# Kernel tuning notes

Measured on AMD Instinct MI355X. Metric: run time of the kernel, lower is better.

Reference implementation:

```python
import jax, jax.numpy as jnp
import numpy as np

# ---- static config (mirrors PointRend init kwargs) ----
H, W = 512, 512          # img_size
CH, CW = 128, 128        # coarse_size
FH, FW = 256, 256        # fine_size
CF = 256                 # fine_channels
NC = 3                   # num_classes (forced by MLP's hard-coded 259/131 channel counts)
NPTS = 2048              # N points
K_OVER = 3               # k oversampling
BELTA = 0.75
NUM_OVER = K_OVER * NPTS          # 6144
STEP1 = int(NPTS * BELTA)         # 1536 uncertain points
STEP2 = NPTS - STEP1              # 512 coverage points


def _xavier(key, c_out, c_in):
    std = (2.0 / (c_in + c_out)) ** 0.5
    return jax.random.normal(key, (c_out, c_in), jnp.float32) * std


def setup_inputs() -> dict:
    key = jax.random.key(0)
    k1, k2, k3, k4, k5, k6 = jax.random.split(key, 6)
    fine_grained = jax.random.normal(k1, (2, CF, FH, FW), jnp.float32)
    coarse_pre = jax.random.normal(k2, (2, NC, CH, CW), jnp.float32)
    # torch.randperm(H*W) done inside forward in the original; passed in for determinism
    random_1d_index = jax.random.permutation(k3, H * W).astype(jnp.int32)
    w1 = _xavier(k4, 256, CF + NC)   # conv1: 1x1, in=259, out=256, no bias
    w2 = _xavier(k5, 128, 256 + 3)   # conv2: in=259, out=128
    w3 = _xavier(k6, NC, 128 + 3)    # conv3: in=131, out=num_classes
    prelu_a = jnp.array(0.25, jnp.float32)  # shared single-param PReLU
    return dict(fine_grained=fine_grained, coarse_pre=coarse_pre,
                w1=w1, w2=w2, w3=w3, prelu_a=prelu_a,
                random_1d_index=random_1d_index)


def _bilinear(x, h, w):
    # matches nn.Upsample(mode='bilinear', align_corners=False)
    return jax.image.resize(x, (x.shape[0], x.shape[1], h, w), method="bilinear")


def _prelu(x, a):
    return jnp.where(x >= 0, x, a * x)


def _mlp(feat, w1, w2, w3, a):
    # feat: [B, N, C] -> channels-first [B, C, N]; BatchNorms in MLP are unused in forward.
    x = jnp.transpose(feat, (0, 2, 1))
    tail = x[:, -3:, :]  # last 3 channels appended to each layer's input
    l1 = _prelu(jnp.einsum('bcn,oc->bon', x, w1), a)
    l2 = _prelu(jnp.einsum('bcn,oc->bon', jnp.concatenate([l1, tail], 1), w2), a)
    return jnp.einsum('bcn,oc->bon', jnp.concatenate([l2, tail], 1), w3)  # [B, NC, N]


def reference(fine_grained, coarse_pre, w1, w2, w3, prelu_a, random_1d_index):
    B = fine_grained.shape[0]
    up_coarse_o = _bilinear(coarse_pre, H, W)            # [B, NC, H, W] logits
    up_coarse_sm = jax.nn.softmax(up_coarse_o, axis=1)   # softmax over classes
    up_fine = _bilinear(fine_grained, H, W)              # [B, CF, H, W]

    h_idx = random_1d_index // W
    w_idx = random_1d_index % W
    all_index = jnp.stack([h_idx, w_idx], axis=1)        # [H*W, 2]
    cand = all_index[:NUM_OVER]                          # oversampled candidates

    # vectorized replacement of the python loop: gather probs at candidates
    over_pre = up_coarse_sm[:, :, cand[:, 0], cand[:, 1]].transpose(0, 2, 1)  # [B, NUM_OVER, NC]
    top2, _ = jax.lax.top_k(over_pre, 2)
    uncertain = 1.0 - (top2[..., 0] - top2[..., 1])      # [B, NUM_OVER]
    _, u_idx = jax.lax.top_k(uncertain, STEP1)           # [B, STEP1]
    u_pts = cand[u_idx]                                  # [B, STEP1, 2]
    cov = jnp.broadcast_to(all_index[-STEP2:][None], (B, STEP2, 2))
    pts = jnp.concatenate([u_pts, cov], axis=1)          # [B, N, 2]

    # masked_select traverses the dense mask in row-major (h,w) order -> sort linear ids
    lin = pts[..., 0] * W + pts[..., 1]                  # [B, N]
    lin_sorted = jnp.sort(lin, axis=1)
    sh, sw = lin_sorted // W, lin_sorted % W
    bidx = jnp.arange(B)[:, None]
    sel_coarse = up_coarse_o[bidx, :, sh, sw]            # [B, N, NC] (pre-softmax feats)
    sel_fine = up_fine[bidx, :, sh, sw]                  # [B, N, CF]

    # faithful to torch: flat concat of the two masked_select outputs, then reshape
    feat = jnp.concatenate([sel_fine.reshape(-1), sel_coarse.reshape(-1)]).reshape(B, NPTS, -1)

    out = _mlp(feat, w1, w2, w3, prelu_a)                # [B, NC, N]
    mask = jnp.zeros((B, H, W), jnp.int32).at[bidx, pts[..., 0], pts[..., 1]].add(1)
    return out, mask
```

## Files before the change

### kernel.cpp

```cpp
#include <hip/hip_runtime.h>

#define NPTS 2048
#define NOVER 6144
#define STEP1 1536
#define STEP2 512
#define HW_TOT 262144

__device__ __forceinline__ float prelu_f(float x, float a) { return x >= 0.0f ? x : a * x; }

__device__ __forceinline__ void coarse_coords(int h, int w, float& fy, float& fx,
                                              int& y0, int& y1, int& x0, int& x1) {
  float sy = (h + 0.5f) * 0.25f - 0.5f;
  float sx = (w + 0.5f) * 0.25f - 0.5f;
  float yf = floorf(sy), xf = floorf(sx);
  fy = sy - yf; fx = sx - xf;
  int yi = (int)yf, xi = (int)xf;
  y0 = min(127, max(0, yi)); y1 = min(127, max(0, yi + 1));
  x0 = min(127, max(0, xi)); x1 = min(127, max(0, xi + 1));
}

__device__ __forceinline__ float coarse_sample(const float* __restrict__ ch, float fy, float fx,
                                               int y0, int y1, int x0, int x1) {
  float v00 = ch[(y0 << 7) + x0];
  float v01 = ch[(y0 << 7) + x1];
  float v10 = ch[(y1 << 7) + x0];
  float v11 = ch[(y1 << 7) + x1];
  return (1.0f - fy) * ((1.0f - fx) * v00 + fx * v01) + fy * ((1.0f - fx) * v10 + fx * v11);
}

__global__ __launch_bounds__(256) void pr_uncfill_v9(uint4* __restrict__ mask4,
                                                     const float* __restrict__ coarse,
                                                     const int* __restrict__ ridx,
                                                     unsigned* __restrict__ keys) {
  const int bb = blockIdx.x;
  if (bb < 512) {
    mask4[bb * 256 + threadIdx.x] = make_uint4(0u, 0u, 0u, 0u);
    return;
  }
  int gid = (bb - 512) * 256 + threadIdx.x;
  if (gid >= 2 * NOVER) return;
  int b = gid / NOVER, i = gid - b * NOVER;
  int lin = ridx[i];
  int h = lin >> 9, w = lin & 511;
  float fy, fx; int y0, y1, x0, x1;
  coarse_coords(h, w, fy, fx, y0, y1, x0, x1);
  const float* cb = coarse + (((size_t)b * 3) << 14);
  float p0 = coarse_sample(cb, fy, fx, y0, y1, x0, x1);
  float p1 = coarse_sample(cb + (1 << 14), fy, fx, y0, y1, x0, x1);
  float p2 = coarse_sample(cb + (2 << 14), fy, fx, y0, y1, x0, x1);
  float m = fmaxf(p0, fmaxf(p1, p2));
  float e0 = expf(p0 - m), e1 = expf(p1 - m), e2 = expf(p2 - m);
  float s = e0 + e1 + e2;
  float q0 = e0 / s, q1 = e1 / s, q2 = e2 / s;
  float a0 = q0, a1 = q1, a2 = q2, tmp;
  if (a0 < a1) { tmp = a0; a0 = a1; a1 = tmp; }
  if (a1 < a2) { tmp = a1; a1 = a2; a2 = tmp; }
  if (a0 < a1) { tmp = a0; a0 = a1; a1 = tmp; }
  float u = 1.0f - (a0 - a1);
  keys[gid] = __float_as_uint(u);
}

__global__ __launch_bounds__(256) void pr_wprep_v4(const float* __restrict__ w1,
                                                   const float* __restrict__ w2,
                                                   float* __restrict__ wT1,
                                                   float* __restrict__ wT2) {
  int gid = blockIdx.x * 256 + threadIdx.x;
  if (gid < 259 * 256) {
    int c = gid >> 8, o = gid & 255;
    wT1[c * 256 + o] = w1[o * 259 + c];
  } else {
    int g2 = gid - 259 * 256;
    if (g2 < 259 * 128) {
      int c = g2 >> 7, o = g2 & 127;
      wT2[c * 128 + o] = w2[o * 259 + c];
    }
  }
}

__global__ __launch_bounds__(1024) void pr_topk_v4(const unsigned* __restrict__ keys,
                                                   const int* __restrict__ ridx,
                                                   int* __restrict__ lin_sorted,
                                                   float* __restrict__ mask) {
  __shared__ unsigned kv[NOVER];
  __shared__ unsigned bitmap[8192];
  __shared__ unsigned hist[256];
  __shared__ unsigned short tiebuf[NOVER];
  __shared__ unsigned scanbuf[16];
  __shared__ unsigned selinfo[2];
  __shared__ int tiecnt;
  const int b = blockIdx.x, t = threadIdx.x;
  const int lane = t & 63, wid = t >> 6;

  for (int i = t; i < NOVER; i += 1024) kv[i] = keys[b * NOVER + i];
  for (int i = t; i < 8192; i += 1024) bitmap[i] = 0u;
  if (t == 0) { selinfo[1] = STEP1; tiecnt = 0; }
  __syncthreads();

  unsigned prefix = 0u;
  for (int pass = 0; pass < 4; ++pass) {
    const int shift = 24 - 8 * pass;
    const unsigned maskHi = (pass == 0) ? 0u : (0xFFFFFFFFu << (shift + 8));
    for (int i = t; i < 256; i += 1024) hist[i] = 0u;
    __syncthreads();
    for (int i = t; i < NOVER; i += 1024) {
      unsigned k = kv[i];
      if ((k & maskHi) == prefix) atomicAdd(&hist[(k >> shift) & 255u], 1u);
    }
    __syncthreads();
    if (t < 64) {
      unsigned h0 = hist[t * 4], h1 = hist[t * 4 + 1], h2 = hist[t * 4 + 2], h3 = hist[t * 4 + 3];
      unsigned q = h0 + h1 + h2 + h3;
      unsigned s = q;
      for (int off = 1; off < 64; off <<= 1) {
        unsigned n = __shfl_down(s, off);
        if (t + off < 64) s += n;
      }
      unsigned exq = s - q;
      unsigned R = selinfo[1];
      unsigned se3 = exq, se2 = se3 + h3, se1 = se2 + h2, se0 = se1 + h1;
      if (se3 < R && R <= se3 + h3)      { selinfo[0] = prefix | ((unsigned)(t * 4 + 3) << shift); selinfo[1] = R - se3; }
      else if (se2 < R && R <= se2 + h2) { selinfo[0] = prefix | ((unsigned)(t * 4 + 2) << shift); selinfo[1] = R - se2; }
      else if (se1 < R && R <= se1 + h1) { selinfo[0] = prefix | ((unsigned)(t * 4 + 1) << shift); selinfo[1] = R - se1; }
      else if (se0 < R && R <= se0 + h0) { selinfo[0] = prefix | ((unsigned)(t * 4 + 0) << shift); selinfo[1] = R - se0; }
    }
    __syncthreads();
    prefix = selinfo[0];
  }
  const unsigned T = prefix;
  const int r = (int)selinfo[1];

  for (int i = t; i < NOVER; i += 1024) {
    unsigned k = kv[i];
    if (k > T) {
      int lin = ridx[i];
      mask[(size_t)b * HW_TOT + lin] = 1.0f;
      atomicOr(&bitmap[lin >> 5], 1u << (lin & 31));
    } else if (k == T) {
      int pos = atomicAdd(&tiecnt, 1);
      tiebuf[pos] = (unsigned short)i;
    }
  }
  for (int i = t; i < STEP2; i += 1024) {
    int lin = ridx[HW_TOT - STEP2 + i];
    mask[(size_t)b * HW_TOT + lin] = 1.0f;
    atomicOr(&bitmap[lin >> 5], 1u << (lin & 31));
  }
  __syncthreads();
  const int m = tiecnt;
  for (int j = t; j < m; j += 1024) {
    int idx = tiebuf[j];
    int rank = 0;
    for (int jj = 0; jj < m; ++jj) rank += (tiebuf[jj] < idx) ? 1 : 0;
    if (rank < r) {
      int lin = ridx[idx];
      mask[(size_t)b * HW_TOT + lin] = 1.0f;
      atomicOr(&bitmap[lin >> 5], 1u << (lin & 31));
    }
  }
  __syncthreads();

  unsigned mySum = 0;
#pragma unroll
  for (int q = 0; q < 8; ++q) mySum += __popc(bitmap[t * 8 + q]);
  unsigned v = mySum;
  for (int off = 1; off < 64; off <<= 1) {
    unsigned n = __shfl_up(v, off);
    if (lane >= off) v += n;
  }
  if (lane == 63) scanbuf[wid] = v;
  __syncthreads();
  if (t == 0) {
    unsigned run = 0;
    for (int w16 = 0; w16 < 16; ++w16) { unsigned tmp = scanbuf[w16]; scanbuf[w16] = run; run += tmp; }
  }
  __syncthreads();
  unsigned pos = (v - mySum) + scanbuf[wid];
  for (int q = 0; q < 8; ++q) {
    unsigned word = bitmap[t * 8 + q];
    int basebit = (t * 8 + q) << 5;
    while (word) {
      int bit = __ffs(word) - 1;
      word &= word - 1;
      lin_sorted[b * NPTS + pos++] = basebit + bit;
    }
  }
}

__global__ __launch_bounds__(256) void pr_gather_v9(const float* __restrict__ fine,
                                                    const float* __restrict__ coarse,
                                                    const int* __restrict__ lin_sorted,
                                                    float* __restrict__ fv,
                                                    float* __restrict__ cv) {
  const int tid = blockIdx.x * 256 + threadIdx.x;
  if (tid < 1048576) {
    const int s = tid & 4095, ch = tid >> 12;
    const int bs = s >> 11;
    const int lin = lin_sorted[s];
    const int h = lin >> 9, w = lin & 511;
    float sy = (h + 0.5f) * 0.5f - 0.5f;
    float sx = (w + 0.5f) * 0.5f - 0.5f;
    float yf = floorf(sy), xf = floorf(sx);
    float fy = sy - yf, fx = sx - xf;
    int yi = (int)yf, xi = (int)xf;
    int y0 = min(255, max(0, yi)), y1 = min(255, max(0, yi + 1));
    int x0 = min(255, max(0, xi)), x1 = min(255, max(0, xi + 1));
    const float* base = fine + (((size_t)(bs * 256 + ch)) << 16);
    float v00 = base[(y0 << 8) + x0];
    float v01 = base[(y0 << 8) + x1];
    float v10 = base[(y1 << 8) + x0];
    float v11 = base[(y1 << 8) + x1];
    fv[tid] = (1.0f - fy) * ((1.0f - fx) * v00 + fx * v01)
            + fy * ((1.0f - fx) * v10 + fx * v11);
  } else {
    const int u = tid - 1048576;
    const int s = u & 4095, kk = u >> 12;
    const int bs = s >> 11;
    const int lin = lin_sorted[s];
    const int h = lin >> 9, w = lin & 511;
    float fy, fx; int y0, y1, x0, x1;
    coarse_coords(h, w, fy, fx, y0, y1, x0, x1);
    cv[u] = coarse_sample(coarse + (((size_t)bs * 3 + kk) << 14), fy, fx, y0, y1, x0, x1);
  }
}

__global__ __launch_bounds__(512) void pr_mlpc_v10(const float* __restrict__ fv,
                                                   const float* __restrict__ cv,
                                                   const float* __restrict__ wT1,
                                                   const float* __restrict__ wT2,
                                                   const float* __restrict__ w3,
                                                   const float* __restrict__ pa,
                                                   float* __restrict__ out) {
  __shared__ __align__(16) float wbuf[2][8192];
  __shared__ __align__(16) float xs[259][16];
  __shared__ __align__(16) float l1p[16][260];
  __shared__ __align__(16) float l2p[16][132];
  const int t = threadIdx.x;
  const int lane = t & 63, wid = t >> 6;
  const int g0 = blockIdx.x * 16;
  const float a = pa[0];

  const int ob1 = ((wid & 3) << 6) + ((lane & 15) << 2);
  const int pp1 = ((wid >> 2) << 3) + ((lane >> 4) << 1);
  const int ob2 = (t & 31) * 4;
  const int pt2 = t >> 5;

  float4 t1[3], t2[3];
#pragma unroll
  for (int i = 0; i < 3; ++i) {
    t1[i] = *(const float4*)&wT1[(256 + i) * 256 + ob1];
    t2[i] = *(const float4*)&wT2[(256 + i) * 128 + ob2];
  }
  float4 st[4];
#pragma unroll
  for (int j = 0; j < 4; ++j) st[j] = *(const float4*)&wT1[(j * 512 + t) * 4];

  for (int task = t; task < 259 * 16; task += 512) {
    int c = task >> 4, p = task & 15;
    int j = (g0 + p) * 259 + c;
    float v;
    if (j < 1048576) {
      v = fv[(j & 255) * 4096 + (j >> 8)];
    } else {
      int jj = j - 1048576;
      int nsrc = jj / 3, kk = jj - nsrc * 3;
      v = cv[kk * 4096 + nsrc];
    }
    xs[c][p] = v;
  }
#pragma unroll
  for (int j = 0; j < 4; ++j) *(float4*)&wbuf[0][(j * 512 + t) * 4] = st[j];
  __syncthreads();

  float acc1[4][2];
#pragma unroll
  for (int i = 0; i < 4; ++i) { acc1[i][0] = 0.0f; acc1[i][1] = 0.0f; }
  float acc2[4] = {0.0f, 0.0f, 0.0f, 0.0f};

  for (int k = 0; k < 12; ++k) {
    const int cur = k & 1;
    if (k < 11) {
      const float* src;
      if (k < 7)       src = wT1 + (k + 1) * 8192;
      else if (k == 7) src = wT2;
      else             src = wT2 + (k - 7) * 8192;
#pragma unroll
      for (int j = 0; j < 4; ++j) st[j] = *(const float4*)&src[(j * 512 + t) * 4];
    }

    if (k < 8) {
      const float* w = wbuf[cur];
      const int c0 = k * 32;
#pragma unroll 8
      for (int cl = 0; cl < 32; ++cl) {
        const float4 wv = *(const float4*)&w[cl * 256 + ob1];
        const float2 xv = *(const float2*)&xs[c0 + cl][pp1];
        acc1[0][0] = fmaf(wv.x, xv.x, acc1[0][0]); acc1[0][1] = fmaf(wv.x, xv.y, acc1[0][1]);
        acc1[1][0] = fmaf(wv.y, xv.x, acc1[1][0]); acc1[1][1] = fmaf(wv.y, xv.y, acc1[1][1]);
        acc1[2][0] = fmaf(wv.z, xv.x, acc1[2][0]); acc1[2][1] = fmaf(wv.z, xv.y, acc1[2][1]);
        acc1[3][0] = fmaf(wv.w, xv.x, acc1[3][0]); acc1[3][1] = fmaf(wv.w, xv.y, acc1[3][1]);
      }
      if (k == 7) {
#pragma unroll
        for (int i = 0; i < 3; ++i) {
          const float2 xv = *(const float2*)&xs[256 + i][pp1];
          acc1[0][0] = fmaf(t1[i].x, xv.x, acc1[0][0]); acc1[0][1] = fmaf(t1[i].x, xv.y, acc1[0][1]);
          acc1[1][0] = fmaf(t1[i].y, xv.x, acc1[1][0]); acc1[1][1] = fmaf(t1[i].y, xv.y, acc1[1][1]);
          acc1[2][0] = fmaf(t1[i].z, xv.x, acc1[2][0]); acc1[2][1] = fmaf(t1[i].z, xv.y, acc1[2][1]);
          acc1[3][0] = fmaf(t1[i].w, xv.x, acc1[3][0]); acc1[3][1] = fmaf(t1[i].w, xv.y, acc1[3][1]);
        }
#pragma unroll
        for (int q = 0; q < 2; ++q) {
          float4 o;
          o.x = prelu_f(acc1[0][q], a);
          o.y = prelu_f(acc1[1][q], a);
          o.z = prelu_f(acc1[2][q], a);
          o.w = prelu_f(acc1[3][q], a);
          *(float4*)&l1p[pp1 + q][ob1] = o;
        }
      }
    } else {
      const float* w = wbuf[cur];
      const int c0 = (k - 8) * 64;
#pragma unroll 4
      for (int cl = 0; cl < 64; cl += 4) {
        const float4 xv = *(const float4*)&l1p[pt2][c0 + cl];
        const float4 w0 = *(const float4*)&w[(cl + 0) * 128 + ob2];
        const float4 w1v = *(const float4*)&w[(cl + 1) * 128 + ob2];
        const float4 w2v = *(const float4*)&w[(cl + 2) * 128 + ob2];
        const float4 w3v = *(const float4*)&w[(cl + 3) * 128 + ob2];
        acc2[0] = fmaf(w0.x, xv.x, acc2[0]); acc2[1] = fmaf(w0.y, xv.x, acc2[1]);
        acc2[2] = fmaf(w0.z, xv.x, acc2[2]); acc2[3] = fmaf(w0.w, xv.x, acc2[3]);
        acc2[0] = fmaf(w1v.x, xv.y, acc2[0]); acc2[1] = fmaf(w1v.y, xv.y, acc2[1]);
        acc2[2] = fmaf(w1v.z, xv.y, acc2[2]); acc2[3] = fmaf(w1v.w, xv.y, acc2[3]);
        acc2[0] = fmaf(w2v.x, xv.z, acc2[0]); acc2[1] = fmaf(w2v.y, xv.z, acc2[1]);
        acc2[2] = fmaf(w2v.z, xv.z, acc2[2]); acc2[3] = fmaf(w2v.w, xv.z, acc2[3]);
        acc2[0] = fmaf(w3v.x, xv.w, acc2[0]); acc2[1] = fmaf(w3v.y, xv.w, acc2[1]);
        acc2[2] = fmaf(w3v.z, xv.w, acc2[2]); acc2[3] = fmaf(w3v.w, xv.w, acc2[3]);
      }
      if (k == 11) {
#pragma unroll
        for (int i = 0; i < 3; ++i) {
          const float x0 = xs[256 + i][pt2];
          acc2[0] = fmaf(t2[i].x, x0, acc2[0]); acc2[1] = fmaf(t2[i].y, x0, acc2[1]);
          acc2[2] = fmaf(t2[i].z, x0, acc2[2]); acc2[3] = fmaf(t2[i].w, x0, acc2[3]);
        }
        float4 o;
        o.x = prelu_f(acc2[0], a);
        o.y = prelu_f(acc2[1], a);
        o.z = prelu_f(acc2[2], a);
        o.w = prelu_f(acc2[3], a);
        *(float4*)&l2p[pt2][ob2] = o;
      }
    }

    if (k < 11) {
#pragma unroll
      for (int j = 0; j < 4; ++j) *(float4*)&wbuf[cur ^ 1][(j * 512 + t) * 4] = st[j];
    }
    __syncthreads();
  }

  if (t < 48) {
    const int o3 = t % 3, p = t / 3;
    const float* wr = w3 + o3 * 131;
    float s = 0.0f;
#pragma unroll 4
    for (int c = 0; c < 128; ++c) s = fmaf(wr[c], l2p[p][c], s);
#pragma unroll
    for (int kk = 0; kk < 3; ++kk) s = fmaf(wr[128 + kk], xs[256 + kk][p], s);
    const int g = g0 + p;
    out[((g >> 11) * 3 + o3) * 2048 + (g & 2047)] = s;
  }
}

extern "C" void kernel_launch(void* const* d_in, const int* in_sizes, int n_in,
                              void* d_out, int out_size, void* d_ws, size_t ws_size,
                              hipStream_t stream) {
  const float* fine   = (const float*)d_in[0];
  const float* coarse = (const float*)d_in[1];
  const float* w1     = (const float*)d_in[2];
  const float* w2     = (const float*)d_in[3];
  const float* w3     = (const float*)d_in[4];
  const float* pa     = (const float*)d_in[5];
  const int*   ridx   = (const int*)d_in[6];

  float* out  = (float*)d_out;
  float* mask = out + 2 * 3 * 2048;

  char* ws = (char*)d_ws;
  int*      lin_sorted = (int*)ws;
  float*    wT1  = (float*)(ws + 16384);
  float*    wT2  = (float*)(ws + 281600);
  unsigned* keys = (unsigned*)(ws + 414208);
  float*    fv   = (float*)(ws + 463360);
  float*    cv   = (float*)(ws + 4657664);

  pr_uncfill_v9<<<560, 256, 0, stream>>>((uint4*)mask, coarse, ridx, keys);
  pr_wprep_v4<<<389, 256, 0, stream>>>(w1, w2, wT1, wT2);
  pr_topk_v4<<<2, 1024, 0, stream>>>(keys, ridx, lin_sorted, mask);
  pr_gather_v9<<<4144, 256, 0, stream>>>(fine, coarse, lin_sorted, fv, cv);
  pr_mlpc_v10<<<256, 512, 0, stream>>>(fv, cv, wT1, wT2, w3, pa, out);
}
```

Before: 280.3 us.

## Fuse bilinear gather into MLP kernel and merge prep kernels

Removes the separate gather kernel and its intermediate fv/cv buffers: the MLP kernel now samples fine and coarse features bilinearly straight into shared memory, with loads batched across 9 iterations per thread to keep many requests in flight. The mask-clear/uncertainty and weight-transpose kernels are merged into a single launch. This drops two launches and a roughly 4 MB write-then-read round trip, but the gather now runs inside only 256 blocks with heavier register use, so memory-level parallelism for the scattered fine-feature reads may be lower.

```diff
diff --git a/kernel.cpp b/kernel.cpp
--- a/kernel.cpp
+++ b/kernel.cpp
@@ -28,43 +28,44 @@
   return (1.0f - fy) * ((1.0f - fx) * v00 + fx * v01) + fy * ((1.0f - fx) * v10 + fx * v11);
 }
 
-__global__ __launch_bounds__(256) void pr_uncfill_v9(uint4* __restrict__ mask4,
-                                                     const float* __restrict__ coarse,
-                                                     const int* __restrict__ ridx,
-                                                     unsigned* __restrict__ keys) {
+__global__ __launch_bounds__(256) void pr_prep_v11(uint4* __restrict__ mask4,
+                                                   const float* __restrict__ coarse,
+                                                   const int* __restrict__ ridx,
+                                                   unsigned* __restrict__ keys,
+                                                   const float* __restrict__ w1,
+                                                   const float* __restrict__ w2,
+                                                   float* __restrict__ wT1,
+                                                   float* __restrict__ wT2) {
   const int bb = blockIdx.x;
   if (bb < 512) {
     mask4[bb * 256 + threadIdx.x] = make_uint4(0u, 0u, 0u, 0u);
     return;
   }
-  int gid = (bb - 512) * 256 + threadIdx.x;
-  if (gid >= 2 * NOVER) return;
-  int b = gid / NOVER, i = gid - b * NOVER;
-  int lin = ridx[i];
-  int h = lin >> 9, w = lin & 511;
-  float fy, fx; int y0, y1, x0, x1;
-  coarse_coords(h, w, fy, fx, y0, y1, x0, x1);
-  const float* cb = coarse + (((size_t)b * 3) << 14);
-  float p0 = coarse_sample(cb, fy, fx, y0, y1, x0, x1);
-  float p1 = coarse_sample(cb + (1 << 14), fy, fx, y0, y1, x0, x1);
-  float p2 = coarse_sample(cb + (2 << 14), fy, fx, y0, y1, x0, x1);
-  float m = fmaxf(p0, fmaxf(p1, p2));
-  float e0 = expf(p0 - m), e1 = expf(p1 - m), e2 = expf(p2 - m);
-  float s = e0 + e1 + e2;
-  float q0 = e0 / s, q1 = e1 / s, q2 = e2 / s;
-  float a0 = q0, a1 = q1, a2 = q2, tmp;
-  if (a0 < a1) { tmp = a0; a0 = a1; a1 = tmp; }
-  if (a1 < a2) { tmp = a1; a1 = a2; a2 = tmp; }
-  if (a0 < a1) { tmp = a0; a0 = a1; a1 = tmp; }
-  float u = 1.0f - (a0 - a1);
-  keys[gid] = __float_as_uint(u);
-}
-
-__global__ __launch_bounds__(256) void pr_wprep_v4(const float* __restrict__ w1,
-                                                   const float* __restrict__ w2,
-                                                   float* __restrict__ wT1,
-                                                   float* __restrict__ wT2) {
-  int gid = blockIdx.x * 256 + threadIdx.x;
+  if (bb < 560) {
+    int gid = (bb - 512) * 256 + threadIdx.x;
+    if (gid >= 2 * NOVER) return;
+    int b = gid / NOVER, i = gid - b * NOVER;
+    int lin = ridx[i];
+    int h = lin >> 9, w = lin & 511;
+    float fy, fx; int y0, y1, x0, x1;
+    coarse_coords(h, w, fy, fx, y0, y1, x0, x1);
+    const float* cb = coarse + (((size_t)b * 3) << 14);
+    float p0 = coarse_sample(cb, fy, fx, y0, y1, x0, x1);
+    float p1 = coarse_sample(cb + (1 << 14), fy, fx, y0, y1, x0, x1);
+    float p2 = coarse_sample(cb + (2 << 14), fy, fx, y0, y1, x0, x1);
+    float m = fmaxf(p0, fmaxf(p1, p2));
+    float e0 = expf(p0 - m), e1 = expf(p1 - m), e2 = expf(p2 - m);
+    float s = e0 + e1 + e2;
+    float q0 = e0 / s, q1 = e1 / s, q2 = e2 / s;
+    float a0 = q0, a1 = q1, a2 = q2, tmp;
+    if (a0 < a1) { tmp = a0; a0 = a1; a1 = tmp; }
+    if (a1 < a2) { tmp = a1; a1 = a2; a2 = tmp; }
+    if (a0 < a1) { tmp = a0; a0 = a1; a1 = tmp; }
+    float u = 1.0f - (a0 - a1);
+    keys[gid] = __float_as_uint(u);
+    return;
+  }
+  int gid = (bb - 560) * 256 + threadIdx.x;
   if (gid < 259 * 256) {
     int c = gid >> 8, o = gid & 255;
     wT1[c * 256 + o] = w1[o * 259 + c];
@@ -186,50 +187,14 @@
   }
 }
 
-__global__ __launch_bounds__(256) void pr_gather_v9(const float* __restrict__ fine,
+__global__ __launch_bounds__(512) void pr_fused_v11(const float* __restrict__ fine,
                                                     const float* __restrict__ coarse,
                                                     const int* __restrict__ lin_sorted,
-                                                    float* __restrict__ fv,
-                                                    float* __restrict__ cv) {
-  const int tid = blockIdx.x * 256 + threadIdx.x;
-  if (tid < 1048576) {
-    const int s = tid & 4095, ch = tid >> 12;
-    const int bs = s >> 11;
-    const int lin = lin_sorted[s];
-    const int h = lin >> 9, w = lin & 511;
-    float sy = (h + 0.5f) * 0.5f - 0.5f;
-    float sx = (w + 0.5f) * 0.5f - 0.5f;
-    float yf = floorf(sy), xf = floorf(sx);
-    float fy = sy - yf, fx = sx - xf;
-    int yi = (int)yf, xi = (int)xf;
-    int y0 = min(255, max(0, yi)), y1 = min(255, max(0, yi + 1));
-    int x0 = min(255, max(0, xi)), x1 = min(255, max(0, xi + 1));
-    const float* base = fine + (((size_t)(bs * 256 + ch)) << 16);
-    float v00 = base[(y0 << 8) + x0];
-    float v01 = base[(y0 << 8) + x1];
-    float v10 = base[(y1 << 8) + x0];
-    float v11 = base[(y1 << 8) + x1];
-    fv[tid] = (1.0f - fy) * ((1.0f - fx) * v00 + fx * v01)
-            + fy * ((1.0f - fx) * v10 + fx * v11);
-  } else {
-    const int u = tid - 1048576;
-    const int s = u & 4095, kk = u >> 12;
-    const int bs = s >> 11;
-    const int lin = lin_sorted[s];
-    const int h = lin >> 9, w = lin & 511;
-    float fy, fx; int y0, y1, x0, x1;
-    coarse_coords(h, w, fy, fx, y0, y1, x0, x1);
-    cv[u] = coarse_sample(coarse + (((size_t)bs * 3 + kk) << 14), fy, fx, y0, y1, x0, x1);
-  }
-}
-
-__global__ __launch_bounds__(512) void pr_mlpc_v10(const float* __restrict__ fv,
-                                                   const float* __restrict__ cv,
-                                                   const float* __restrict__ wT1,
-                                                   const float* __restrict__ wT2,
-                                                   const float* __restrict__ w3,
-                                                   const float* __restrict__ pa,
-                                                   float* __restrict__ out) {
+                                                    const float* __restrict__ wT1,
+                                                    const float* __restrict__ wT2,
+                                                    const float* __restrict__ w3,
+                                                    const float* __restrict__ pa,
+                                                    float* __restrict__ out) {
   __shared__ __align__(16) float wbuf[2][8192];
   __shared__ __align__(16) float xs[259][16];
   __shared__ __align__(16) float l1p[16][260];
@@ -254,18 +219,56 @@
 #pragma unroll
   for (int j = 0; j < 4; ++j) st[j] = *(const float4*)&wT1[(j * 512 + t) * 4];
 
-  for (int task = t; task < 259 * 16; task += 512) {
-    int c = task >> 4, p = task & 15;
-    int j = (g0 + p) * 259 + c;
-    float v;
-    if (j < 1048576) {
-      v = fv[(j & 255) * 4096 + (j >> 8)];
-    } else {
-      int jj = j - 1048576;
-      int nsrc = jj / 3, kk = jj - nsrc * 3;
-      v = cv[kk * 4096 + nsrc];
-    }
-    xs[c][p] = v;
+  float v00[9], v01[9], v10[9], v11[9], gfy[9], gfx[9];
+#pragma unroll
+  for (int it = 0; it < 9; ++it) {
+    const int task = t + it * 512;
+    if (task < 4144) {
+      const int c = task >> 4, p = task & 15;
+      const int j = (g0 + p) * 259 + c;
+      if (j < 1048576) {
+        const int nsrc = j >> 8, ch = j & 255;
+        const int bs = nsrc >> 11;
+        const int lin = lin_sorted[nsrc];
+        const int h = lin >> 9, w = lin & 511;
+        float sy = (h + 0.5f) * 0.5f - 0.5f;
+        float sx = (w + 0.5f) * 0.5f - 0.5f;
+        float yf = floorf(sy), xf = floorf(sx);
+        gfy[it] = sy - yf; gfx[it] = sx - xf;
+        int yi = (int)yf, xi = (int)xf;
+        int y0 = min(255, max(0, yi)), y1 = min(255, max(0, yi + 1));
+        int x0 = min(255, max(0, xi)), x1 = min(255, max(0, xi + 1));
+        const float* base = fine + (((size_t)(bs * 256 + ch)) << 16);
+        v00[it] = base[(y0 << 8) + x0];
+        v01[it] = base[(y0 << 8) + x1];
+        v10[it] = base[(y1 << 8) + x0];
+        v11[it] = base[(y1 << 8) + x1];
+      } else {
+        const int jj = j - 1048576;
+        const int nsrc = jj / 3, kk = jj - nsrc * 3;
+        const int bs = nsrc >> 11;
+        const int lin = lin_sorted[nsrc];
+        const int h = lin >> 9, w = lin & 511;
+        float fy, fx; int y0, y1, x0, x1;
+        coarse_coords(h, w, fy, fx, y0, y1, x0, x1);
+        gfy[it] = fy; gfx[it] = fx;
+        const float* cb = coarse + (((size_t)bs * 3 + kk) << 14);
+        v00[it] = cb[(y0 << 7) + x0];
+        v01[it] = cb[(y0 << 7) + x1];
+        v10[it] = cb[(y1 << 7) + x0];
+        v11[it] = cb[(y1 << 7) + x1];
+      }
+    }
+  }
+#pragma unroll
+  for (int it = 0; it < 9; ++it) {
+    const int task = t + it * 512;
+    if (task < 4144) {
+      const int c = task >> 4, p = task & 15;
+      const float fy = gfy[it], fx = gfx[it];
+      xs[c][p] = (1.0f - fy) * ((1.0f - fx) * v00[it] + fx * v01[it])
+               + fy * ((1.0f - fx) * v10[it] + fx * v11[it]);
+    }
   }
 #pragma unroll
   for (int j = 0; j < 4; ++j) *(float4*)&wbuf[0][(j * 512 + t) * 4] = st[j];
@@ -392,12 +395,8 @@
   float*    wT1  = (float*)(ws + 16384);
   float*    wT2  = (float*)(ws + 281600);
   unsigned* keys = (unsigned*)(ws + 414208);
-  float*    fv   = (float*)(ws + 463360);
-  float*    cv   = (float*)(ws + 4657664);
-
-  pr_uncfill_v9<<<560, 256, 0, stream>>>((uint4*)mask, coarse, ridx, keys);
-  pr_wprep_v4<<<389, 256, 0, stream>>>(w1, w2, wT1, wT2);
+
+  pr_prep_v11<<<949, 256, 0, stream>>>((uint4*)mask, coarse, ridx, keys, w1, w2, wT1, wT2);
   pr_topk_v4<<<2, 1024, 0, stream>>>(keys, ridx, lin_sorted, mask);
-  pr_gather_v9<<<4144, 256, 0, stream>>>(fine, coarse, lin_sorted, fv, cv);
-  pr_mlpc_v10<<<256, 512, 0, stream>>>(fv, cv, wT1, wT2, w3, pa, out);
-}
+  pr_fused_v11<<<256, 512, 0, stream>>>(fine, coarse, lin_sorted, wT1, wT2, w3, pa, out);
+}
```

New measurement: 262.8 us. 1.07x faster.
